# Performance work log

Hardware: AMD Instinct MI355X
Metric: run time of the kernel (lower is better)

Reference implementation:

```python
import jax, jax.numpy as jnp
import numpy as np

B = 4096
D = 128
TEMP = 0.5
EPS = 1e-8  # torch cosine_similarity norm clamp


def setup_inputs() -> dict:
    key = jax.random.key(0)
    k1, k2 = jax.random.split(key)
    zi = jax.random.normal(k1, (B, D), dtype=jnp.float32)
    zj = jax.random.normal(k2, (B, D), dtype=jnp.float32)
    return {"zi": zi, "zj": zj}


def reference(zi, zj):
    b = zi.shape[0]
    n2 = 2 * b
    z = jnp.concatenate([zi, zj], axis=0)                      # (2N, D)
    norm = jnp.maximum(jnp.linalg.norm(z, axis=-1, keepdims=True), EPS)
    zn = z / norm
    sim = zn @ zn.T                                            # (2N, 2N) cosine similarity
    # positives: torch.diag(sim, +B) and torch.diag(sim, -B)
    right = jnp.diagonal(sim, offset=b)                        # sim[i, i+B]
    left = jnp.diagonal(sim, offset=-b)                        # sim[i+B, i]
    pos = jnp.concatenate([left, right]) / TEMP                # (2N,)
    # logits row i = [pos_i] + all sims except self-diagonal and the positive,
    # so the softmax denominator set = all entries except the self-diagonal.
    logits = sim / TEMP
    neg_big = jnp.asarray(jnp.finfo(logits.dtype).min, logits.dtype)
    masked = jnp.where(jnp.eye(n2, dtype=bool), neg_big, logits)
    lse = jax.nn.logsumexp(masked, axis=1)                     # (2N,)
    # CrossEntropyLoss(reduction='sum') with label 0, then / 2N
    loss = jnp.sum(lse - pos) / n2
    return loss
```

## Files before the change

### kernel.cpp

```cpp
#include <hip/hip_runtime.h>
#include <hip/hip_bf16.h>


#define BB 4096
#define N2 8192
#define DD 128
#define CSPLIT 16
#define CW (N2 / CSPLIT)
#define NCT (CW / 16)

using bf16 = __hip_bfloat16;
typedef __attribute__((ext_vector_type(8))) short short8;
typedef __attribute__((ext_vector_type(4))) float float4v;

__global__ __launch_bounds__(256) void ntx_norm_kernel(
    const float* __restrict__ zi, const float* __restrict__ zj,
    bf16* __restrict__ zn, float* __restrict__ rowsum, float* __restrict__ pos) {
  const int wave = threadIdx.x >> 6;
  const int lane = threadIdx.x & 63;
  const int row = blockIdx.x * 4 + wave;
  const float* own = (row < BB) ? (zi + (size_t)row * DD)
                                : (zj + (size_t)(row - BB) * DD);
  const float* par = (row < BB) ? (zj + (size_t)row * DD)
                                : (zi + (size_t)(row - BB) * DD);
  float2 v = ((const float2*)own)[lane];
  float2 w = ((const float2*)par)[lane];
  float s1 = v.x * v.x + v.y * v.y;
  float s2 = w.x * w.x + w.y * w.y;
  float s3 = v.x * w.x + v.y * w.y;
  #pragma unroll
  for (int o = 32; o > 0; o >>= 1) {
    s1 += __shfl_xor(s1, o);
    s2 += __shfl_xor(s2, o);
    s3 += __shfl_xor(s3, o);
  }
  float nv = fmaxf(sqrtf(s1), 1e-8f);
  float nw = fmaxf(sqrtf(s2), 1e-8f);
  float rv = 1.0f / nv;
  bf16 bx = __float2bfloat16(v.x * rv);
  bf16 by = __float2bfloat16(v.y * rv);
  __hip_bfloat162 h2; h2.x = bx; h2.y = by;
  ((__hip_bfloat162*)(zn + (size_t)row * DD))[lane] = h2;
  float fx = __bfloat162float(bx), fy = __bfloat162float(by);
  float sii = fx * fx + fy * fy;
  #pragma unroll
  for (int o = 32; o > 0; o >>= 1) sii += __shfl_xor(sii, o);
  if (lane == 0) {
    rowsum[row] = -__expf(2.0f * sii);
    pos[row] = s3 / (nv * nw);
  }
}

__global__ __launch_bounds__(256) void ntx_sim_kernel(
    const bf16* __restrict__ zn, float* __restrict__ rowsum) {
  const int wave = threadIdx.x >> 6;
  const int lane = threadIdx.x & 63;
  const int quad = lane >> 4;
  const int l15  = lane & 15;
  const short* zs = (const short*)zn;

  const int rowBase = blockIdx.y * 256 + wave * 64;
  const int colBase0 = blockIdx.x * CW;

  short8 a[4][4];
  #pragma unroll
  for (int t = 0; t < 4; t++) {
    const short* ap = zs + (size_t)(rowBase + t * 16 + l15) * DD + quad * 8;
    #pragma unroll
    for (int c = 0; c < 4; c++) a[t][c] = *(const short8*)(ap + c * 32);
  }

  float rs[4][4];
  #pragma unroll
  for (int t = 0; t < 4; t++)
    #pragma unroll
    for (int r = 0; r < 4; r++) rs[t][r] = 0.0f;

  const short* bbase = zs + (size_t)(colBase0 + l15) * DD + quad * 8;

  short8 b[4];
  #pragma unroll
  for (int c = 0; c < 4; c++) b[c] = *(const short8*)(bbase + c * 32);

  for (int ct = 0; ct < NCT; ct++) {
    const int nct = (ct + 1) & (NCT - 1);
    const short* bp = bbase + (size_t)nct * 16 * DD;
    short8 bn[4];
    #pragma unroll
    for (int c = 0; c < 4; c++) bn[c] = *(const short8*)(bp + c * 32);

    #pragma unroll
    for (int t = 0; t < 4; t++) {
      float4v acc = {0.f, 0.f, 0.f, 0.f};
      acc = __builtin_amdgcn_mfma_f32_16x16x32_bf16(a[t][0], b[0], acc, 0, 0, 0);
      acc = __builtin_amdgcn_mfma_f32_16x16x32_bf16(a[t][1], b[1], acc, 0, 0, 0);
      acc = __builtin_amdgcn_mfma_f32_16x16x32_bf16(a[t][2], b[2], acc, 0, 0, 0);
      acc = __builtin_amdgcn_mfma_f32_16x16x32_bf16(a[t][3], b[3], acc, 0, 0, 0);
      #pragma unroll
      for (int r = 0; r < 4; r++) rs[t][r] += __expf(acc[r] * 2.0f);
    }

    #pragma unroll
    for (int c = 0; c < 4; c++) b[c] = bn[c];
  }

  #pragma unroll
  for (int t = 0; t < 4; t++) {
    #pragma unroll
    for (int r = 0; r < 4; r++) {
      float s = rs[t][r];
      s += __shfl_xor(s, 1);
      s += __shfl_xor(s, 2);
      s += __shfl_xor(s, 4);
      s += __shfl_xor(s, 8);
      if (l15 == 0)
        atomicAdd(&rowsum[rowBase + t * 16 + quad * 4 + r], s);
    }
  }
}

__global__ __launch_bounds__(1024) void ntx_finalize_kernel(
    const float* __restrict__ rowsum, const float* __restrict__ pos,
    float* __restrict__ out) {
  float s = 0.f;
  for (int i = threadIdx.x; i < N2; i += 1024)
    s += __logf(rowsum[i]) - 2.0f * pos[i];
  #pragma unroll
  for (int o = 32; o > 0; o >>= 1) s += __shfl_xor(s, o);
  __shared__ float sm[16];
  const int wave = threadIdx.x >> 6;
  const int lane = threadIdx.x & 63;
  if (lane == 0) sm[wave] = s;
  __syncthreads();
  if (threadIdx.x == 0) {
    float t = 0.f;
    #pragma unroll
    for (int i = 0; i < 16; i++) t += sm[i];
    out[0] = t / (float)N2;
  }
}

extern "C" void kernel_launch(void* const* d_in, const int* in_sizes, int n_in,
                              void* d_out, int out_size, void* d_ws, size_t ws_size,
                              hipStream_t stream) {
  const float* zi = (const float*)d_in[0];
  const float* zj = (const float*)d_in[1];
  float* out = (float*)d_out;

  char* ws = (char*)d_ws;
  bf16* zn = (bf16*)ws;
  float* rowsum = (float*)(ws + (size_t)N2 * DD * 2);
  float* pos = rowsum + N2;

  ntx_norm_kernel<<<N2 / 4, 256, 0, stream>>>(zi, zj, zn, rowsum, pos);
  dim3 grid(CSPLIT, N2 / 256);
  ntx_sim_kernel<<<grid, 256, 0, stream>>>(zn, rowsum);
  ntx_finalize_kernel<<<1, 1024, 0, stream>>>(rowsum, pos, out);
}
```

Before: 100.6 us.

## Double-buffer B tiles, use exp2 directly, raise column split and occupancy hint

The similarity kernel now ping-pongs between two register buffers for the B column tiles, so no register copy is needed each iteration and the load of the next tile overlaps with the current MFMA work. The exponential is computed directly with exp2 and a pre-folded 2*log2(e) constant instead of __expf(x*2). The column split doubles to 32, giving twice as many blocks but twice as many atomics per row. A launch bound requesting 4 blocks per CU is added to raise occupancy, at the risk of register spills.

New measurement: 393.6 us. +291.2%, slower.

```diff
diff --git a/kernel.cpp b/kernel.cpp
--- a/kernel.cpp
+++ b/kernel.cpp
@@ -5,13 +5,15 @@
 #define BB 4096
 #define N2 8192
 #define DD 128
-#define CSPLIT 16
+#define CSPLIT 32
 #define CW (N2 / CSPLIT)
 #define NCT (CW / 16)
 
 using bf16 = __hip_bfloat16;
 typedef __attribute__((ext_vector_type(8))) short short8;
 typedef __attribute__((ext_vector_type(4))) float float4v;
+
+#define TWO_LOG2E 2.8853900817779268f
 
 __global__ __launch_bounds__(256) void ntx_norm_kernel(
     const float* __restrict__ zi, const float* __restrict__ zj,
@@ -51,7 +53,7 @@
   }
 }
 
-__global__ __launch_bounds__(256) void ntx_sim_kernel(
+__global__ __launch_bounds__(256, 4) void ntx_sim_kernel(
     const bf16* __restrict__ zn, float* __restrict__ rowsum) {
   const int wave = threadIdx.x >> 6;
   const int lane = threadIdx.x & 63;
@@ -78,31 +80,36 @@
 
   const short* bbase = zs + (size_t)(colBase0 + l15) * DD + quad * 8;
 
-  short8 b[4];
+  short8 b0[4], b1[4];
   #pragma unroll
-  for (int c = 0; c < 4; c++) b[c] = *(const short8*)(bbase + c * 32);
+  for (int c = 0; c < 4; c++) b0[c] = *(const short8*)(bbase + c * 32);
 
-  for (int ct = 0; ct < NCT; ct++) {
-    const int nct = (ct + 1) & (NCT - 1);
-    const short* bp = bbase + (size_t)nct * 16 * DD;
-    short8 bn[4];
+#define COMPUTE_TILE(BUF)                                                     \
+  do {                                                                        \
+    _Pragma("unroll")                                                         \
+    for (int t = 0; t < 4; t++) {                                             \
+      float4v acc = {0.f, 0.f, 0.f, 0.f};                                     \
+      acc = __builtin_amdgcn_mfma_f32_16x16x32_bf16(a[t][0], BUF[0], acc, 0, 0, 0); \
+      acc = __builtin_amdgcn_mfma_f32_16x16x32_bf16(a[t][1], BUF[1], acc, 0, 0, 0); \
+      acc = __builtin_amdgcn_mfma_f32_16x16x32_bf16(a[t][2], BUF[2], acc, 0, 0, 0); \
+      acc = __builtin_amdgcn_mfma_f32_16x16x32_bf16(a[t][3], BUF[3], acc, 0, 0, 0); \
+      _Pragma("unroll")                                                       \
+      for (int r = 0; r < 4; r++)                                             \
+        rs[t][r] += __builtin_exp2f(acc[r] * TWO_LOG2E);                      \
+    }                                                                         \
+  } while (0)
+
+  for (int ct = 0; ct < NCT; ct += 2) {
+    const short* bp1 = bbase + (size_t)((ct + 1) & (NCT - 1)) * 16 * DD;
     #pragma unroll
-    for (int c = 0; c < 4; c++) bn[c] = *(const short8*)(bp + c * 32);
-
+    for (int c = 0; c < 4; c++) b1[c] = *(const short8*)(bp1 + c * 32);
+    COMPUTE_TILE(b0);
+    const short* bp0 = bbase + (size_t)((ct + 2) & (NCT - 1)) * 16 * DD;
     #pragma unroll
-    for (int t = 0; t < 4; t++) {
-      float4v acc = {0.f, 0.f, 0.f, 0.f};
-      acc = __builtin_amdgcn_mfma_f32_16x16x32_bf16(a[t][0], b[0], acc, 0, 0, 0);
-      acc = __builtin_amdgcn_mfma_f32_16x16x32_bf16(a[t][1], b[1], acc, 0, 0, 0);
-      acc = __builtin_amdgcn_mfma_f32_16x16x32_bf16(a[t][2], b[2], acc, 0, 0, 0);
-      acc = __builtin_amdgcn_mfma_f32_16x16x32_bf16(a[t][3], b[3], acc, 0, 0, 0);
-      #pragma unroll
-      for (int r = 0; r < 4; r++) rs[t][r] += __expf(acc[r] * 2.0f);
-    }
-
-    #pragma unroll
-    for (int c = 0; c < 4; c++) b[c] = bn[c];
+    for (int c = 0; c < 4; c++) b0[c] = *(const short8*)(bp0 + c * 32);
+    COMPUTE_TILE(b1);
   }
+#undef COMPUTE_TILE
 
   #pragma unroll
   for (int t = 0; t < 4; t++) {
```

## Stage column tiles in swizzled LDS and prescale rows to use exp2

Applied to the files above, without the earlier changes.

The sim kernel now copies its whole 128-column B tile into LDS once per block using direct global-to-LDS loads with an XOR swizzle, and reads B fragments from LDS instead of global memory. The column split grows from 16 to 64, so each block covers fewer columns and the grid has more blocks. The norm kernel writes a second copy of the normalized rows scaled by 2*log2(e), so the sim kernel can use a bare exp2 instead of a multiply followed by exp. This adds a second bf16 buffer and extra quantization from rounding the scaled values, and it means four times as many atomic adds to rowsum.

Measured after the change: 101.7 us. About the same (+1.0%).

```diff
diff --git a/kernel.cpp b/kernel.cpp
--- a/kernel.cpp
+++ b/kernel.cpp
@@ -1,21 +1,31 @@
 #include <hip/hip_runtime.h>
 #include <hip/hip_bf16.h>
+#include <stdint.h>
 
 
 #define BB 4096
 #define N2 8192
 #define DD 128
-#define CSPLIT 16
+#define CSPLIT 64
 #define CW (N2 / CSPLIT)
 #define NCT (CW / 16)
+#define TWO_LOG2E 2.8853900817779268f
 
 using bf16 = __hip_bfloat16;
 typedef __attribute__((ext_vector_type(8))) short short8;
 typedef __attribute__((ext_vector_type(4))) float float4v;
 
+__device__ inline void load_lds16(const void* g, void* l) {
+  __builtin_amdgcn_global_load_lds(
+      (const __attribute__((address_space(1))) uint32_t*)g,
+      (__attribute__((address_space(3))) uint32_t*)(uint32_t)(uintptr_t)l,
+      16, 0, 0);
+}
+
 __global__ __launch_bounds__(256) void ntx_norm_kernel(
     const float* __restrict__ zi, const float* __restrict__ zj,
-    bf16* __restrict__ zn, float* __restrict__ rowsum, float* __restrict__ pos) {
+    bf16* __restrict__ zn, bf16* __restrict__ zn_s,
+    float* __restrict__ rowsum, float* __restrict__ pos) {
   const int wave = threadIdx.x >> 6;
   const int lane = threadIdx.x & 63;
   const int row = blockIdx.x * 4 + wave;
@@ -39,33 +49,51 @@
   float rv = 1.0f / nv;
   bf16 bx = __float2bfloat16(v.x * rv);
   bf16 by = __float2bfloat16(v.y * rv);
+  bf16 sx = __float2bfloat16(v.x * rv * TWO_LOG2E);
+  bf16 sy = __float2bfloat16(v.y * rv * TWO_LOG2E);
   __hip_bfloat162 h2; h2.x = bx; h2.y = by;
   ((__hip_bfloat162*)(zn + (size_t)row * DD))[lane] = h2;
-  float fx = __bfloat162float(bx), fy = __bfloat162float(by);
-  float sii = fx * fx + fy * fy;
+  __hip_bfloat162 g2; g2.x = sx; g2.y = sy;
+  ((__hip_bfloat162*)(zn_s + (size_t)row * DD))[lane] = g2;
+  float sii = __bfloat162float(sx) * __bfloat162float(bx) +
+              __bfloat162float(sy) * __bfloat162float(by);
   #pragma unroll
   for (int o = 32; o > 0; o >>= 1) sii += __shfl_xor(sii, o);
   if (lane == 0) {
-    rowsum[row] = -__expf(2.0f * sii);
+    rowsum[row] = -__builtin_amdgcn_exp2f(sii);
     pos[row] = s3 / (nv * nw);
   }
 }
 
 __global__ __launch_bounds__(256) void ntx_sim_kernel(
-    const bf16* __restrict__ zn, float* __restrict__ rowsum) {
-  const int wave = threadIdx.x >> 6;
-  const int lane = threadIdx.x & 63;
+    const short* __restrict__ zn, const short* __restrict__ zn_s,
+    float* __restrict__ rowsum) {
+  __shared__ short lds[CW * DD];
+  const int tid  = threadIdx.x;
+  const int wave = tid >> 6;
+  const int lane = tid & 63;
   const int quad = lane >> 4;
   const int l15  = lane & 15;
-  const short* zs = (const short*)zn;
 
-  const int rowBase = blockIdx.y * 256 + wave * 64;
+  const int rowBase  = blockIdx.y * 256 + wave * 64;
   const int colBase0 = blockIdx.x * CW;
+
+  {
+    const int swz = (tid & 15) ^ (tid >> 4);
+    const char* gbase = (const char*)zn + ((size_t)colBase0 << 8);
+    char* lbase = (char*)lds;
+    #pragma unroll
+    for (int j = 0; j < 8; j++) {
+      const int lr = j * 16 + (tid >> 4);
+      load_lds16(gbase + ((size_t)lr << 8) + (swz << 4),
+                 lbase + j * 4096 + tid * 16);
+    }
+  }
 
   short8 a[4][4];
   #pragma unroll
   for (int t = 0; t < 4; t++) {
-    const short* ap = zs + (size_t)(rowBase + t * 16 + l15) * DD + quad * 8;
+    const short* ap = zn_s + (size_t)(rowBase + t * 16 + l15) * DD + quad * 8;
     #pragma unroll
     for (int c = 0; c < 4; c++) a[t][c] = *(const short8*)(ap + c * 32);
   }
@@ -76,19 +104,16 @@
     #pragma unroll
     for (int r = 0; r < 4; r++) rs[t][r] = 0.0f;
 
-  const short* bbase = zs + (size_t)(colBase0 + l15) * DD + quad * 8;
+  __syncthreads();
 
-  short8 b[4];
-  #pragma unroll
-  for (int c = 0; c < 4; c++) b[c] = *(const short8*)(bbase + c * 32);
-
+  #pragma unroll 2
   for (int ct = 0; ct < NCT; ct++) {
-    const int nct = (ct + 1) & (NCT - 1);
-    const short* bp = bbase + (size_t)nct * 16 * DD;
-    short8 bn[4];
+    short8 b[4];
     #pragma unroll
-    for (int c = 0; c < 4; c++) bn[c] = *(const short8*)(bp + c * 32);
-
+    for (int kc = 0; kc < 4; kc++) {
+      const int off = (ct * 16 + l15) * DD + (((kc * 4 + quad) ^ l15) << 3);
+      b[kc] = *(const short8*)(lds + off);
+    }
     #pragma unroll
     for (int t = 0; t < 4; t++) {
       float4v acc = {0.f, 0.f, 0.f, 0.f};
@@ -97,11 +122,9 @@
       acc = __builtin_amdgcn_mfma_f32_16x16x32_bf16(a[t][2], b[2], acc, 0, 0, 0);
       acc = __builtin_amdgcn_mfma_f32_16x16x32_bf16(a[t][3], b[3], acc, 0, 0, 0);
       #pragma unroll
-      for (int r = 0; r < 4; r++) rs[t][r] += __expf(acc[r] * 2.0f);
+      for (int r = 0; r < 4; r++)
+        rs[t][r] += __builtin_amdgcn_exp2f(acc[r]);
     }
-
-    #pragma unroll
-    for (int c = 0; c < 4; c++) b[c] = bn[c];
   }
 
   #pragma unroll
@@ -148,12 +171,14 @@
   float* out = (float*)d_out;
 
   char* ws = (char*)d_ws;
-  bf16* zn = (bf16*)ws;
-  float* rowsum = (float*)(ws + (size_t)N2 * DD * 2);
+  bf16* zn   = (bf16*)ws;
+  bf16* zn_s = (bf16*)(ws + (size_t)N2 * DD * 2);
+  float* rowsum = (float*)(ws + 2 * (size_t)N2 * DD * 2);
   float* pos = rowsum + N2;
 
-  ntx_norm_kernel<<<N2 / 4, 256, 0, stream>>>(zi, zj, zn, rowsum, pos);
+  ntx_norm_kernel<<<N2 / 4, 256, 0, stream>>>(zi, zj, zn, zn_s, rowsum, pos);
   dim3 grid(CSPLIT, N2 / 256);
-  ntx_sim_kernel<<<grid, 256, 0, stream>>>(zn, rowsum);
+  ntx_sim_kernel<<<grid, 256, 0, stream>>>((const short*)zn, (const short*)zn_s,
+                                           rowsum);
   ntx_finalize_kernel<<<1, 1024, 0, stream>>>(rowsum, pos, out);
 }
```
